# Kernel optimization log

Measured on AMD Instinct MI355X. Metric: run time of the kernel, lower is better.

## Reference

```python
import jax, jax.numpy as jnp
import numpy as np

E, NB, F, H = 30, 12, 1024, 32  # numEmotions, numBasicEmotions, numCommonFeatures, hidden
EPS = 1e-12  # F.normalize eps


def setup_inputs() -> dict:
    key = jax.random.key(0)
    ks = jax.random.split(key, 7)
    B, L = 8192, 128
    return {
        "basicEmotionDistributions": jax.random.uniform(ks[0], (B, NB, L), dtype=jnp.float32),
        "encodedFeatures": jax.random.normal(ks[1], (B, F), dtype=jnp.float32),
        "allBasicEmotionWeights": jax.random.normal(ks[2], (E, 1, NB, 1), dtype=jnp.float32),
        "W1": jax.random.normal(ks[3], (E, F, H), dtype=jnp.float32) / np.sqrt(F),
        "b1": jax.random.normal(ks[4], (E, H), dtype=jnp.float32) * 0.01,
        "W2": jax.random.normal(ks[5], (E, H, NB), dtype=jnp.float32) / np.sqrt(H),
        "b2": jax.random.normal(ks[6], (E, NB), dtype=jnp.float32) * 0.01,
    }


def reference(basicEmotionDistributions, encodedFeatures, allBasicEmotionWeights, W1, b1, W2, b2):
    # L1-normalize exp(weights) along basic-emotion dim: (E, NB)
    ew = jnp.exp(allBasicEmotionWeights[:, 0, :, 0])  # (E, NB)
    allW = ew / jnp.maximum(jnp.sum(jnp.abs(ew), axis=1, keepdims=True), EPS)

    # Batched per-emotion 2-layer MLP: (E, B, NB)
    h = jax.nn.selu(jnp.einsum('bf,efh->ebh', encodedFeatures, W1) + b1[:, None, :])
    mlp = jnp.einsum('ebh,ehn->ebn', h, W2) + b2[:, None, :]

    # updated weights and signed L1 normalization over NB dim
    updated = allW[:, None, :] + mlp  # (E, B, NB)
    # sign(x) * normalize(|x|, p=1) == x / max(sum|x|, eps)
    w = updated / jnp.maximum(jnp.sum(jnp.abs(updated), axis=2, keepdims=True), EPS)

    # weighted sum over basic emotions, then softmax over emotion length
    mixed = jnp.einsum('ebn,bnl->ebl', w, basicEmotionDistributions)  # (E, B, L)
    return jax.nn.softmax(mixed, axis=2)
```

## Files before the change

kernel.cpp:

```cpp
#include <hip/hip_runtime.h>

typedef __attribute__((ext_vector_type(8))) _Float16 half8;
typedef __attribute__((ext_vector_type(4))) float f32x4;

#define GAS(p) ((const __attribute__((address_space(1))) void*)(p))
#define LAS(p) ((__attribute__((address_space(3))) void*)(p))

__global__ __launch_bounds__(256) void cvt_pre(const float* __restrict__ feat,
                                               const float* __restrict__ W1,
                                               _Float16* __restrict__ A16,
                                               _Float16* __restrict__ W1T) {
    if (blockIdx.x < 4096) {
        int gid = blockIdx.x * 256 + threadIdx.x;
        int k8   = gid & 3;
        int m    = (gid >> 2) & 15;
        int frag = gid >> 6;
        int mf = frag & 7;
        int kc = (frag >> 3) & 31;
        int bt = frag >> 8;
        int b  = bt * 128 + mf * 16 + m;
        int f0 = kc * 32 + k8 * 8;
        const float4* src = (const float4*)(feat + (size_t)b * 1024 + f0);
        float4 v0 = src[0], v1 = src[1];
        half8 o;
        o[0] = (_Float16)v0.x; o[1] = (_Float16)v0.y;
        o[2] = (_Float16)v0.z; o[3] = (_Float16)v0.w;
        o[4] = (_Float16)v1.x; o[5] = (_Float16)v1.y;
        o[6] = (_Float16)v1.z; o[7] = (_Float16)v1.w;
        *(half8*)(A16 + ((size_t)frag * 64 + k8 * 16 + m) * 8) = o;
    } else {
        int gid = (blockIdx.x - 4096) * 256 + threadIdx.x;
        int k8   = gid & 3;
        int n    = (gid >> 2) & 15;
        int frag = gid >> 6;
        int nf = frag & 1;
        int kc = (frag >> 1) & 31;
        int e  = frag >> 6;
        int h  = nf * 16 + n;
        int f0 = kc * 32 + k8 * 8;
        const float* src = W1 + ((size_t)e * 1024 + f0) * 32 + h;
        half8 o;
#pragma unroll
        for (int j = 0; j < 8; ++j) o[j] = (_Float16)src[j * 32];
        *(half8*)(W1T + ((size_t)frag * 64 + k8 * 16 + n) * 8) = o;
    }
}

__global__ __launch_bounds__(256) void gemm_mlp(
    const _Float16* __restrict__ A16, const _Float16* __restrict__ W1T,
    const float* __restrict__ b1, const float* __restrict__ W2,
    const float* __restrict__ b2, const float* __restrict__ wts,
    float* __restrict__ wbuf) {
    __shared__ __align__(16) unsigned char smem[28672];
    unsigned char* Ash = smem;
    unsigned char* Bsh = smem + 16384;
    float* w2s = (float*)(smem + 24576);
    float* cb2 = (float*)(smem + 27648);
    float* ews = cb2 + 24;
    float* h_sh = (float*)smem;

    const int tid = threadIdx.x;
    const int e0 = blockIdx.x * 2;
    const int bt = blockIdx.y;
    const int w  = tid >> 6, l = tid & 63;
    const int q  = l >> 4, lc = l & 15;

    for (int i = tid; i < 768; i += 256) w2s[i] = W2[e0 * 384 + i];
    if (tid < 24) {
        cb2[tid] = b2[e0 * 12 + tid];
        ews[tid] = __expf(wts[e0 * 12 + tid]);
    }

    const _Float16* Abase = A16 + (size_t)bt * 131072;
    const _Float16* Bbase = W1T + (size_t)e0 * 32768;

    f32x4 zero = {0.f, 0.f, 0.f, 0.f};
    f32x4 acc[2][4];
#pragma unroll
    for (int i = 0; i < 2; ++i)
#pragma unroll
        for (int j = 0; j < 4; ++j) acc[i][j] = zero;

    for (int it = 0; it < 16; ++it) {
        const _Float16* Ait = Abase + it * 8192;
#pragma unroll
        for (int i = 0; i < 4; ++i) {
            int s = w * 4 + i;
            __builtin_amdgcn_global_load_lds(GAS(Ait + s * 512 + l * 8),
                                             LAS(Ash + s * 1024), 16, 0, 0);
        }
#pragma unroll
        for (int j = 0; j < 2; ++j) {
            int f  = w * 2 + j;
            int be = f >> 2, kn = f & 3;
            __builtin_amdgcn_global_load_lds(
                GAS(Bbase + be * 32768 + it * 2048 + kn * 512 + l * 8),
                LAS(Bsh + f * 1024), 16, 0, 0);
        }
        __syncthreads();
#pragma unroll
        for (int kc2 = 0; kc2 < 2; ++kc2) {
            half8 a0  = *(half8*)(Ash + (kc2 * 8 + 2 * w + 0) * 1024 + l * 16);
            half8 a1  = *(half8*)(Ash + (kc2 * 8 + 2 * w + 1) * 1024 + l * 16);
            half8 b00 = *(half8*)(Bsh + (0 + kc2 * 2 + 0) * 1024 + l * 16);
            half8 b01 = *(half8*)(Bsh + (0 + kc2 * 2 + 1) * 1024 + l * 16);
            half8 b10 = *(half8*)(Bsh + (4 + kc2 * 2 + 0) * 1024 + l * 16);
            half8 b11 = *(half8*)(Bsh + (4 + kc2 * 2 + 1) * 1024 + l * 16);
            acc[0][0] = __builtin_amdgcn_mfma_f32_16x16x32_f16(a0, b00, acc[0][0], 0, 0, 0);
            acc[0][1] = __builtin_amdgcn_mfma_f32_16x16x32_f16(a0, b01, acc[0][1], 0, 0, 0);
            acc[0][2] = __builtin_amdgcn_mfma_f32_16x16x32_f16(a0, b10, acc[0][2], 0, 0, 0);
            acc[0][3] = __builtin_amdgcn_mfma_f32_16x16x32_f16(a0, b11, acc[0][3], 0, 0, 0);
            acc[1][0] = __builtin_amdgcn_mfma_f32_16x16x32_f16(a1, b00, acc[1][0], 0, 0, 0);
            acc[1][1] = __builtin_amdgcn_mfma_f32_16x16x32_f16(a1, b01, acc[1][1], 0, 0, 0);
            acc[1][2] = __builtin_amdgcn_mfma_f32_16x16x32_f16(a1, b10, acc[1][2], 0, 0, 0);
            acc[1][3] = __builtin_amdgcn_mfma_f32_16x16x32_f16(a1, b11, acc[1][3], 0, 0, 0);
        }
        __syncthreads();
    }

    const float SC = 1.0507009873554805f, AL = 1.6732632423543772f;
    const int m2 = tid >> 1, sub = tid & 1;

#pragma unroll
    for (int eo = 0; eo < 2; ++eo) {
        const float b1a = b1[(e0 + eo) * 32 + lc];
        const float b1b = b1[(e0 + eo) * 32 + 16 + lc];
#pragma unroll
        for (int mf = 0; mf < 2; ++mf)
#pragma unroll
            for (int nf = 0; nf < 2; ++nf)
#pragma unroll
                for (int r = 0; r < 4; ++r) {
                    int m   = w * 32 + mf * 16 + q * 4 + r;
                    int col = nf * 16 + lc;
                    float x = acc[mf][eo * 2 + nf][r] + (nf ? b1b : b1a);
                    float hv = x > 0.f ? SC * x : SC * AL * (__expf(x) - 1.f);
                    h_sh[m * 33 + col] = hv;
                }
        __syncthreads();

        float u[6] = {0.f, 0.f, 0.f, 0.f, 0.f, 0.f};
        const float* hrow = h_sh + m2 * 33;
        const float* wbase = w2s + eo * 384 + sub * 6;
#pragma unroll 8
        for (int h = 0; h < 32; ++h) {
            float hv = hrow[h];
            const float* wr = wbase + h * 12;
#pragma unroll
            for (int j = 0; j < 6; ++j) u[j] += hv * wr[j];
        }
        float sew = 0.f;
#pragma unroll
        for (int i = 0; i < 12; ++i) sew += ews[eo * 12 + i];
        sew = fmaxf(sew, 1e-12f);
        float sabs = 0.f;
#pragma unroll
        for (int j = 0; j < 6; ++j) {
            u[j] += cb2[eo * 12 + sub * 6 + j] + ews[eo * 12 + sub * 6 + j] / sew;
            sabs += fabsf(u[j]);
        }
        sabs += __shfl_xor(sabs, 1);
        float inv = 1.f / fmaxf(sabs, 1e-12f);
        int b = bt * 128 + m2;
        float* dst = wbuf + (size_t)(e0 + eo) * 98304 + b * 12 + sub * 6;
#pragma unroll
        for (int j = 0; j < 6; ++j) dst[j] = u[j] * inv;
        __syncthreads();
    }
}

__global__ __launch_bounds__(256) void mix_softmax(
    const float* __restrict__ dist, const float* __restrict__ wbuf,
    float* __restrict__ out) {
    __shared__ float wsm[8 * 360];
    const int tid = threadIdx.x;
    const int b0 = blockIdx.x * 8;
    for (int i = tid; i < 2880; i += 256) {
        int e = i / 96, r = i - e * 96;
        wsm[(r / 12) * 360 + e * 12 + (r % 12)] = wbuf[(size_t)e * 98304 + b0 * 12 + r];
    }
    __syncthreads();
    const int m = tid >> 5, l4 = tid & 31;
    const int b = b0 + m;
    const float* dbase = dist + (size_t)b * 1536 + l4 * 4;
    f32x4 d[12];
#pragma unroll
    for (int n = 0; n < 12; ++n) d[n] = *(const f32x4*)(dbase + n * 128);
    const float* wrow = wsm + m * 360;
    for (int e = 0; e < 30; ++e) {
        const float* wr = wrow + e * 12;
        f32x4 a = {0.f, 0.f, 0.f, 0.f};
#pragma unroll
        for (int n = 0; n < 12; ++n) a += wr[n] * d[n];
        f32x4 ex;
        ex[0] = __expf(a[0]); ex[1] = __expf(a[1]);
        ex[2] = __expf(a[2]); ex[3] = __expf(a[3]);
        float sm = ex[0] + ex[1] + ex[2] + ex[3];
#pragma unroll
        for (int s = 16; s >= 1; s >>= 1) sm += __shfl_xor(sm, s);
        f32x4 o = ex * (1.f / sm);
        *(f32x4*)(out + ((size_t)e * 8192 + b) * 128 + l4 * 4) = o;
    }
}

extern "C" void kernel_launch(void* const* d_in, const int* in_sizes, int n_in,
                              void* d_out, int out_size, void* d_ws, size_t ws_size,
                              hipStream_t stream) {
    const float* dist = (const float*)d_in[0];
    const float* feat = (const float*)d_in[1];
    const float* wts  = (const float*)d_in[2];
    const float* W1   = (const float*)d_in[3];
    const float* b1   = (const float*)d_in[4];
    const float* W2   = (const float*)d_in[5];
    const float* b2   = (const float*)d_in[6];
    float* out = (float*)d_out;

    _Float16* A16 = (_Float16*)d_ws;
    _Float16* W1T = (_Float16*)((char*)d_ws + 16777216);
    float*   wbuf = (float*)((char*)d_ws + 16777216 + 1966080);

    cvt_pre<<<4576, 256, 0, stream>>>(feat, W1, A16, W1T);
    dim3 g1(15, 64);
    gemm_mlp<<<g1, 256, 0, stream>>>(A16, W1T, b1, W2, b2, wts, wbuf);
    mix_softmax<<<1024, 256, 0, stream>>>(dist, wbuf, out);
}
```

Before: 253.4 us.

## Process four emotions per GEMM block with a 2x2 wave tile

Measured after the change: 260.4 us. 1.03x slower.

```diff
diff --git a/kernel.cpp b/kernel.cpp
--- a/kernel.cpp
+++ b/kernel.cpp
@@ -51,33 +51,37 @@
     const float* __restrict__ b1, const float* __restrict__ W2,
     const float* __restrict__ b2, const float* __restrict__ wts,
     float* __restrict__ wbuf) {
-    __shared__ __align__(16) unsigned char smem[28672];
+    __shared__ __align__(16) unsigned char smem[39296];
     unsigned char* Ash = smem;
     unsigned char* Bsh = smem + 16384;
-    float* w2s = (float*)(smem + 24576);
-    float* cb2 = (float*)(smem + 27648);
-    float* ews = cb2 + 24;
     float* h_sh = (float*)smem;
+    float* w2s = (float*)(smem + 32768);
+    float* cb2 = (float*)(smem + 32768 + 6144);
+    float* ews = cb2 + 48;
 
     const int tid = threadIdx.x;
-    const int e0 = blockIdx.x * 2;
+    const int e0 = blockIdx.x * 4;
     const int bt = blockIdx.y;
     const int w  = tid >> 6, l = tid & 63;
     const int q  = l >> 4, lc = l & 15;
-
-    for (int i = tid; i < 768; i += 256) w2s[i] = W2[e0 * 384 + i];
-    if (tid < 24) {
-        cb2[tid] = b2[e0 * 12 + tid];
-        ews[tid] = __expf(wts[e0 * 12 + tid]);
+    const int wm = w & 1, wn = w >> 1;
+
+    for (int i = tid; i < 1536; i += 256) {
+        int ee = e0 + i / 384; if (ee >= 30) ee = 0;
+        w2s[i] = W2[ee * 384 + (i % 384)];
+    }
+    if (tid < 48) {
+        int ee = e0 + tid / 12; if (ee >= 30) ee = 0;
+        cb2[tid] = b2[ee * 12 + (tid % 12)];
+        ews[tid] = __expf(wts[ee * 12 + (tid % 12)]);
     }
 
     const _Float16* Abase = A16 + (size_t)bt * 131072;
-    const _Float16* Bbase = W1T + (size_t)e0 * 32768;
 
     f32x4 zero = {0.f, 0.f, 0.f, 0.f};
-    f32x4 acc[2][4];
-#pragma unroll
-    for (int i = 0; i < 2; ++i)
+    f32x4 acc[4][4];
+#pragma unroll
+    for (int i = 0; i < 4; ++i)
 #pragma unroll
         for (int j = 0; j < 4; ++j) acc[i][j] = zero;
 
@@ -85,35 +89,34 @@
         const _Float16* Ait = Abase + it * 8192;
 #pragma unroll
         for (int i = 0; i < 4; ++i) {
-            int s = w * 4 + i;
-            __builtin_amdgcn_global_load_lds(GAS(Ait + s * 512 + l * 8),
-                                             LAS(Ash + s * 1024), 16, 0, 0);
-        }
-#pragma unroll
-        for (int j = 0; j < 2; ++j) {
-            int f  = w * 2 + j;
-            int be = f >> 2, kn = f & 3;
+            int f = w * 4 + i;
+            __builtin_amdgcn_global_load_lds(GAS(Ait + f * 512 + l * 8),
+                                             LAS(Ash + f * 1024), 16, 0, 0);
+        }
+#pragma unroll
+        for (int i = 0; i < 4; ++i) {
+            int f = w * 4 + i;
+            int kc2 = f >> 3, sub = f & 7, eo = sub >> 1, nf = sub & 1;
             __builtin_amdgcn_global_load_lds(
-                GAS(Bbase + be * 32768 + it * 2048 + kn * 512 + l * 8),
+                GAS(W1T + ((size_t)(e0 + eo) * 64 + (2 * it + kc2) * 2 + nf) * 512 + l * 8),
                 LAS(Bsh + f * 1024), 16, 0, 0);
         }
         __syncthreads();
 #pragma unroll
         for (int kc2 = 0; kc2 < 2; ++kc2) {
-            half8 a0  = *(half8*)(Ash + (kc2 * 8 + 2 * w + 0) * 1024 + l * 16);
-            half8 a1  = *(half8*)(Ash + (kc2 * 8 + 2 * w + 1) * 1024 + l * 16);
-            half8 b00 = *(half8*)(Bsh + (0 + kc2 * 2 + 0) * 1024 + l * 16);
-            half8 b01 = *(half8*)(Bsh + (0 + kc2 * 2 + 1) * 1024 + l * 16);
-            half8 b10 = *(half8*)(Bsh + (4 + kc2 * 2 + 0) * 1024 + l * 16);
-            half8 b11 = *(half8*)(Bsh + (4 + kc2 * 2 + 1) * 1024 + l * 16);
-            acc[0][0] = __builtin_amdgcn_mfma_f32_16x16x32_f16(a0, b00, acc[0][0], 0, 0, 0);
-            acc[0][1] = __builtin_amdgcn_mfma_f32_16x16x32_f16(a0, b01, acc[0][1], 0, 0, 0);
-            acc[0][2] = __builtin_amdgcn_mfma_f32_16x16x32_f16(a0, b10, acc[0][2], 0, 0, 0);
-            acc[0][3] = __builtin_amdgcn_mfma_f32_16x16x32_f16(a0, b11, acc[0][3], 0, 0, 0);
-            acc[1][0] = __builtin_amdgcn_mfma_f32_16x16x32_f16(a1, b00, acc[1][0], 0, 0, 0);
-            acc[1][1] = __builtin_amdgcn_mfma_f32_16x16x32_f16(a1, b01, acc[1][1], 0, 0, 0);
-            acc[1][2] = __builtin_amdgcn_mfma_f32_16x16x32_f16(a1, b10, acc[1][2], 0, 0, 0);
-            acc[1][3] = __builtin_amdgcn_mfma_f32_16x16x32_f16(a1, b11, acc[1][3], 0, 0, 0);
+            half8 a[4], bv[4];
+#pragma unroll
+            for (int mf = 0; mf < 4; ++mf)
+                a[mf] = *(half8*)(Ash + (kc2 * 8 + wm * 4 + mf) * 1024 + l * 16);
+#pragma unroll
+            for (int nf = 0; nf < 4; ++nf)
+                bv[nf] = *(half8*)(Bsh + (kc2 * 8 + wn * 4 + nf) * 1024 + l * 16);
+#pragma unroll
+            for (int mf = 0; mf < 4; ++mf)
+#pragma unroll
+                for (int nf = 0; nf < 4; ++nf)
+                    acc[mf][nf] = __builtin_amdgcn_mfma_f32_16x16x32_f16(
+                        a[mf], bv[nf], acc[mf][nf], 0, 0, 0);
         }
         __syncthreads();
     }
@@ -122,21 +125,25 @@
     const int m2 = tid >> 1, sub = tid & 1;
 
 #pragma unroll
-    for (int eo = 0; eo < 2; ++eo) {
-        const float b1a = b1[(e0 + eo) * 32 + lc];
-        const float b1b = b1[(e0 + eo) * 32 + 16 + lc];
-#pragma unroll
-        for (int mf = 0; mf < 2; ++mf)
-#pragma unroll
-            for (int nf = 0; nf < 2; ++nf)
-#pragma unroll
-                for (int r = 0; r < 4; ++r) {
-                    int m   = w * 32 + mf * 16 + q * 4 + r;
-                    int col = nf * 16 + lc;
-                    float x = acc[mf][eo * 2 + nf][r] + (nf ? b1b : b1a);
-                    float hv = x > 0.f ? SC * x : SC * AL * (__expf(x) - 1.f);
-                    h_sh[m * 33 + col] = hv;
-                }
+    for (int eo = 0; eo < 4; ++eo) {
+        int ec = (e0 + eo < 30) ? e0 + eo : 0;
+        if (wn == (eo >> 1)) {
+            int nf0 = (eo & 1) * 2;
+#pragma unroll
+            for (int j = 0; j < 2; ++j) {
+                float b1v = b1[ec * 32 + j * 16 + lc];
+#pragma unroll
+                for (int mf = 0; mf < 4; ++mf)
+#pragma unroll
+                    for (int r = 0; r < 4; ++r) {
+                        int m   = wm * 64 + mf * 16 + q * 4 + r;
+                        int col = j * 16 + lc;
+                        float x = acc[mf][nf0 + j][r] + b1v;
+                        float hv = x > 0.f ? SC * x : SC * AL * (__expf(x) - 1.f);
+                        h_sh[m * 33 + col] = hv;
+                    }
+            }
+        }
         __syncthreads();
 
         float u[6] = {0.f, 0.f, 0.f, 0.f, 0.f, 0.f};
@@ -161,10 +168,12 @@
         }
         sabs += __shfl_xor(sabs, 1);
         float inv = 1.f / fmaxf(sabs, 1e-12f);
-        int b = bt * 128 + m2;
-        float* dst = wbuf + (size_t)(e0 + eo) * 98304 + b * 12 + sub * 6;
-#pragma unroll
-        for (int j = 0; j < 6; ++j) dst[j] = u[j] * inv;
+        if (e0 + eo < 30) {
+            int b = bt * 128 + m2;
+            float* dst = wbuf + (size_t)(e0 + eo) * 98304 + b * 12 + sub * 6;
+#pragma unroll
+            for (int j = 0; j < 6; ++j) dst[j] = u[j] * inv;
+        }
         __syncthreads();
     }
 }
@@ -217,10 +226,10 @@
 
     _Float16* A16 = (_Float16*)d_ws;
     _Float16* W1T = (_Float16*)((char*)d_ws + 16777216);
-    float*   wbuf = (float*)((char*)d_ws + 16777216 + 1966080);
+    float*   wbuf = (float*)((char*)d_ws + 16777216 + 4194304);
 
     cvt_pre<<<4576, 256, 0, stream>>>(feat, W1, A16, W1T);
-    dim3 g1(15, 64);
+    dim3 g1(8, 64);
     gemm_mlp<<<g1, 256, 0, stream>>>(A16, W1T, b1, W2, b2, wts, wbuf);
     mix_softmax<<<1024, 256, 0, stream>>>(dist, wbuf, out);
 }
```
